# Kernel tuning notes

Hardware: AMD Instinct MI355X
Metric: run time of the kernel (lower is better)

The kernel has to match this reference:

```python
import jax, jax.numpy as jnp
import numpy as np

D_MODEL = 1024
H = 8        # num_heads_kv
G = 8        # num_groups_q (must equal H for the original matmul to be valid)
DEPTH = D_MODEL // H  # 128, depth_q == depth_kv
NEG_INF = jnp.float32(-1e9)


def setup_inputs() -> dict:
    key = jax.random.key(0)
    ks = jax.random.split(key, 7)
    B, Lq, Lk = 2, 2048, 2048
    w_scale = 0.02
    return {
        "x_q": jax.random.normal(ks[0], (B, Lq, D_MODEL), jnp.float32),
        "x_k": jax.random.normal(ks[1], (B, Lk, D_MODEL), jnp.float32),
        "x_v": jax.random.normal(ks[2], (B, Lk, D_MODEL), jnp.float32),
        "Wq": jax.random.normal(ks[3], (D_MODEL, D_MODEL), jnp.float32) * w_scale,
        "Wk": jax.random.normal(ks[4], (D_MODEL, D_MODEL), jnp.float32) * w_scale,
        "Wv": jax.random.normal(ks[5], (D_MODEL, D_MODEL), jnp.float32) * w_scale,
        "Wo": jax.random.normal(ks[6], (D_MODEL, D_MODEL), jnp.float32) * w_scale,
        "mask": jnp.ones((B, 1, Lq, Lk), jnp.bool_),
    }


def reference(x_q, x_k, x_v, Wq, Wk, Wv, Wo, mask):
    B, Lq, _ = x_q.shape
    Lk = x_k.shape[1]
    # nn.Linear: y = x @ W.T (no bias)
    q = (x_q @ Wq.T).reshape(B, Lq, G, DEPTH).transpose(0, 2, 1, 3)  # (B,G,Lq,D)
    k = (x_k @ Wk.T).reshape(B, Lk, H, DEPTH).transpose(0, 2, 1, 3)  # (B,H,Lk,D)
    v = (x_v @ Wv.T).reshape(B, Lk, H, DEPTH).transpose(0, 2, 1, 3)  # (B,H,Lk,D)
    scale = 1.0 / np.sqrt(DEPTH).astype(np.float32)

    def attend(q_g):  # q_g: (B,Lq,D), one query group broadcast over all KV heads
        s = jnp.einsum("bqd,bhkd->bhqk", q_g, k) * scale       # (B,H,Lq,Lk)
        s = jnp.where(mask, s, NEG_INF)                          # masked_fill(mask==0, -inf)
        w = jax.nn.softmax(s, axis=-1)
        o = jnp.einsum("bhqk,bhkd->bhqd", w, v)                 # (B,H,Lq,D)
        return o.mean(axis=1)                                    # mean over kv heads -> (B,Lq,D)

    # sequential over groups (matches original Python loop; bounds peak memory)
    out_g = jax.lax.map(attend, jnp.moveaxis(q, 1, 0))           # (G,B,Lq,D)
    combined = jnp.moveaxis(out_g, 0, 2).reshape(B, Lq, G * DEPTH)
    return combined @ Wo.T
```

## Files before the change

### kernel.cpp

```cpp
#include <hip/hip_runtime.h>
#include <type_traits>
#include <utility>


using u16 = unsigned short;

typedef float f32x4 __attribute__((ext_vector_type(4)));
typedef short short8 __attribute__((ext_vector_type(8)));
typedef __bf16 bf16x8 __attribute__((ext_vector_type(8)));

#define DEV __device__ __forceinline__

template <typename V, typename = void> struct MfmaTakes : std::false_type {};
template <typename V>
struct MfmaTakes<V, std::void_t<decltype(__builtin_amdgcn_mfma_f32_16x16x32_bf16(
    std::declval<V>(), std::declval<V>(), std::declval<f32x4>(), 0, 0, 0))>>
    : std::true_type {};
using mfma_ab = std::conditional_t<MfmaTakes<short8>::value, short8, bf16x8>;
static_assert(sizeof(mfma_ab) == 16, "mfma operand must be 4 VGPRs");

DEV f32x4 mfma16x16(short8 a, short8 b, f32x4 c) {
  return __builtin_amdgcn_mfma_f32_16x16x32_bf16(
      __builtin_bit_cast(mfma_ab, a), __builtin_bit_cast(mfma_ab, b), c, 0, 0, 0);
}

DEV u16 f2b(float f) {
  unsigned u = __float_as_uint(f);
  u += 0x7fffu + ((u >> 16) & 1u);
  return (u16)(u >> 16);
}
DEV float b2f(u16 h) { return __uint_as_float(((unsigned)h) << 16); }

DEV short8 ld8(const u16* p) { return *reinterpret_cast<const short8*>(p); }
DEV void st8(u16* p, short8 v) { *reinterpret_cast<short8*>(p) = v; }

__global__ __launch_bounds__(256) void k_cvt(const float* __restrict__ src,
                                             u16* __restrict__ dst, int n4) {
  int i = blockIdx.x * 256 + threadIdx.x;
  if (i >= n4) return;
  float4 v = reinterpret_cast<const float4*>(src)[i];
  unsigned long long r = (unsigned long long)f2b(v.x) |
                         ((unsigned long long)f2b(v.y) << 16) |
                         ((unsigned long long)f2b(v.z) << 32) |
                         ((unsigned long long)f2b(v.w) << 48);
  reinterpret_cast<unsigned long long*>(dst)[i] = r;
}

template <typename AT, typename OutT>
__global__ __launch_bounds__(256) void k_gemm_nt(const AT* __restrict__ A,
                                                 const u16* __restrict__ Bm,
                                                 OutT* __restrict__ C,
                                                 int M, int N, int K) {
  __shared__ __align__(16) u16 As[128][40];
  __shared__ __align__(16) u16 Bs[128][40];
  const int tid = threadIdx.x, lane = tid & 63, w = tid >> 6;
  const int lr = lane & 15, lg = lane >> 4;
  const int wr = w >> 1, wc = w & 1;
  const int m0 = blockIdx.y * 128, n0 = blockIdx.x * 128;

  f32x4 acc[4][4];
#pragma unroll
  for (int mi = 0; mi < 4; ++mi)
#pragma unroll
    for (int ni = 0; ni < 4; ++ni) acc[mi][ni] = f32x4{0.f, 0.f, 0.f, 0.f};

  for (int k0 = 0; k0 < K; k0 += 32) {
#pragma unroll
    for (int i = 0; i < 2; ++i) {
      int c = tid + i * 256;
      int r = c >> 2, j = c & 3;
      short8 va;
      if constexpr (std::is_same_v<AT, float>) {
        const float* ap = A + (size_t)(m0 + r) * K + k0 + j * 8;
        float4 f0 = *reinterpret_cast<const float4*>(ap);
        float4 f1 = *reinterpret_cast<const float4*>(ap + 4);
        va = short8{(short)f2b(f0.x), (short)f2b(f0.y), (short)f2b(f0.z), (short)f2b(f0.w),
                    (short)f2b(f1.x), (short)f2b(f1.y), (short)f2b(f1.z), (short)f2b(f1.w)};
      } else {
        va = ld8(A + (size_t)(m0 + r) * K + k0 + j * 8);
      }
      short8 vb = ld8(Bm + (size_t)(n0 + r) * K + k0 + j * 8);
      st8(&As[r][j * 8], va);
      st8(&Bs[r][j * 8], vb);
    }
    __syncthreads();
    short8 af[4], bf[4];
#pragma unroll
    for (int mi = 0; mi < 4; ++mi) af[mi] = ld8(&As[wr * 64 + mi * 16 + lr][lg * 8]);
#pragma unroll
    for (int ni = 0; ni < 4; ++ni) bf[ni] = ld8(&Bs[wc * 64 + ni * 16 + lr][lg * 8]);
#pragma unroll
    for (int mi = 0; mi < 4; ++mi)
#pragma unroll
      for (int ni = 0; ni < 4; ++ni)
        acc[mi][ni] = mfma16x16(af[mi], bf[ni], acc[mi][ni]);
    __syncthreads();
  }
#pragma unroll
  for (int mi = 0; mi < 4; ++mi)
#pragma unroll
    for (int ni = 0; ni < 4; ++ni)
#pragma unroll
      for (int r = 0; r < 4; ++r) {
        int row = m0 + wr * 64 + mi * 16 + lg * 4 + r;
        int col = n0 + wc * 64 + ni * 16 + lr;
        if constexpr (std::is_same_v<OutT, float>)
          C[(size_t)row * N + col] = acc[mi][ni][r];
        else
          C[(size_t)row * N + col] = f2b(acc[mi][ni][r]);
      }
}

__global__ __launch_bounds__(256) void k_transpose_v(const u16* __restrict__ V,
                                                     u16* __restrict__ Vt) {
  int bid = blockIdx.x;
  int lt = bid & 31, dt = (bid >> 5) & 1, bh = bid >> 6;
  int b = bh >> 3, h = bh & 7;
  __shared__ u16 t[64][72];
#pragma unroll
  for (int i = 0; i < 16; ++i) {
    int idx = threadIdx.x + i * 256;
    int r = idx >> 6, c = idx & 63;
    t[r][c] = V[(size_t)(b * 2048 + lt * 64 + r) * 1024 + h * 128 + dt * 64 + c];
  }
  __syncthreads();
#pragma unroll
  for (int i = 0; i < 16; ++i) {
    int idx = threadIdx.x + i * 256;
    int r = idx >> 6, c = idx & 63;
    Vt[(size_t)(bh * 128 + dt * 64 + r) * 2048 + lt * 64 + c] = t[c][r];
  }
}

__global__ __launch_bounds__(256) void k_attn(const u16* __restrict__ Q,
                                              const u16* __restrict__ K,
                                              const u16* __restrict__ Vt,
                                              float* __restrict__ Cacc) {
  const int bid = blockIdx.x;
  const int qt = bid & 31, g = (bid >> 5) & 7, b = (bid >> 8) & 1, h = (bid >> 9) & 7;
  const int tid = threadIdx.x, lane = tid & 63, w = tid >> 6;
  const int lr = lane & 15, lg = lane >> 4;

  __shared__ __align__(16) u16 ks[64 * 128];
  __shared__ __align__(16) u16 vts[128 * 64];
  __shared__ __align__(16) u16 ps[4 * 16 * 64];

  auto KS = [&](int row, int e) -> u16* { return &ks[row * 128 + (e ^ ((row & 7) << 3))]; };
  auto VT = [&](int row, int e) -> u16* { return &vts[row * 64 + (e ^ ((row & 7) << 3))]; };
  auto PS = [&](int ww, int row, int e) -> u16* {
    return &ps[ww * 1024 + row * 64 + (e ^ ((row & 7) << 3))];
  };

  const int q0 = qt * 64;

  short8 qf[4];
  {
    const u16* qp = Q + (size_t)(b * 2048 + q0 + w * 16 + lr) * 1024 + g * 128;
    const float sc = 0.08838834764831845f;
#pragma unroll
    for (int kf = 0; kf < 4; ++kf) {
      short8 v = ld8(qp + kf * 32 + lg * 8);
#pragma unroll
      for (int e = 0; e < 8; ++e) v[e] = (short)f2b(b2f((u16)v[e]) * sc);
      qf[kf] = v;
    }
  }

  const short one_bf = (short)0x3F80;
  const short8 ones = short8{one_bf, one_bf, one_bf, one_bf, one_bf, one_bf, one_bf, one_bf};

  f32x4 oh[8];
#pragma unroll
  for (int f = 0; f < 8; ++f) oh[f] = f32x4{0.f, 0.f, 0.f, 0.f};
  f32x4 lsum = f32x4{0.f, 0.f, 0.f, 0.f};
  float mrun[4] = {-1e30f, -1e30f, -1e30f, -1e30f};

  for (int kt = 0; kt < 32; ++kt) {
    const int k0 = kt * 64;
#pragma unroll
    for (int i = 0; i < 4; ++i) {
      int c = tid + i * 256;
      {
        int r = c >> 4, j = c & 15;
        st8(KS(r, j * 8), ld8(K + (size_t)(b * 2048 + k0 + r) * 1024 + h * 128 + j * 8));
      }
      {
        int d = c >> 3, j = c & 7;
        st8(VT(d, j * 8), ld8(Vt + (size_t)((b * 8 + h) * 128 + d) * 2048 + k0 + j * 8));
      }
    }
    __syncthreads();

    f32x4 s[4];
#pragma unroll
    for (int c = 0; c < 4; ++c) {
      s[c] = f32x4{0.f, 0.f, 0.f, 0.f};
#pragma unroll
      for (int kf = 0; kf < 4; ++kf) {
        short8 bfr = ld8(KS(c * 16 + lr, kf * 32 + lg * 8));
        s[c] = mfma16x16(qf[kf], bfr, s[c]);
      }
    }

    float vmax[4];
    bool grow = false;
#pragma unroll
    for (int r = 0; r < 4; ++r) {
      float v = fmaxf(fmaxf(s[0][r], s[1][r]), fmaxf(s[2][r], s[3][r]));
#pragma unroll
      for (int off = 1; off <= 8; off <<= 1) v = fmaxf(v, __shfl_xor(v, off));
      vmax[r] = v;
      grow = grow || (v > mrun[r]);
    }
    if (__any(grow)) {
#pragma unroll
      for (int r = 0; r < 4; ++r) {
        float mn = fmaxf(mrun[r], vmax[r]);
        float corr = __expf(mrun[r] - mn);
        mrun[r] = mn;
        lsum[r] *= corr;
#pragma unroll
        for (int f = 0; f < 8; ++f) oh[f][r] *= corr;
      }
    }
#pragma unroll
    for (int c = 0; c < 4; ++c)
#pragma unroll
      for (int r = 0; r < 4; ++r) {
        float p = __expf(s[c][r] - mrun[r]);
        *PS(w, lg * 4 + r, c * 16 + lr) = __builtin_bit_cast(u16, (__bf16)p);
      }
    asm volatile("s_waitcnt lgkmcnt(0)" ::: "memory");
    __builtin_amdgcn_sched_barrier(0);

    short8 p0 = ld8(PS(w, lr, lg * 8));
    short8 p1 = ld8(PS(w, lr, 32 + lg * 8));
    lsum = mfma16x16(p0, ones, lsum);
    lsum = mfma16x16(p1, ones, lsum);
#pragma unroll
    for (int f = 0; f < 8; ++f) {
      short8 v0 = ld8(VT(f * 16 + lr, lg * 8));
      short8 v1 = ld8(VT(f * 16 + lr, 32 + lg * 8));
      oh[f] = mfma16x16(p0, v0, oh[f]);
      oh[f] = mfma16x16(p1, v1, oh[f]);
    }
    __syncthreads();
  }

  float norm[4];
#pragma unroll
  for (int r = 0; r < 4; ++r) norm[r] = 0.125f / lsum[r];
  float* co = Cacc + (size_t)(b * 2048 + q0 + w * 16 + lg * 4) * 1024 + g * 128 + lr;
#pragma unroll
  for (int f = 0; f < 8; ++f)
#pragma unroll
    for (int r = 0; r < 4; ++r)
      atomicAdd(&co[(size_t)r * 1024 + f * 16], oh[f][r] * norm[r]);
}

extern "C" void kernel_launch(void* const* d_in, const int* in_sizes, int n_in,
                              void* d_out, int out_size, void* d_ws, size_t ws_size,
                              hipStream_t stream) {
  const float* x_q = (const float*)d_in[0];
  const float* x_k = (const float*)d_in[1];
  const float* x_v = (const float*)d_in[2];
  const float* Wq = (const float*)d_in[3];
  const float* Wk = (const float*)d_in[4];
  const float* Wv = (const float*)d_in[5];
  const float* Wo = (const float*)d_in[6];
  float* out = (float*)d_out;

  const size_t NX = (size_t)2 * 2048 * 1024;
  const size_t NW = (size_t)1024 * 1024;
  u16* ws = (u16*)d_ws;
  u16* xqb = ws;
  u16* xkb = xqb + NX;
  u16* xvb = xkb + NX;
  u16* wqb = xvb + NX;
  u16* wkb = wqb + NW;
  u16* wvb = wkb + NW;
  u16* wob = wvb + NW;
  u16* Qb  = wob + NW;
  u16* Kb  = Qb + NX;
  u16* Vb  = Kb + NX;
  u16* Vtb = xqb;
  float* Cacc = (float*)xkb;

  dim3 blk(256);
  k_cvt<<<dim3(NX / 1024), blk, 0, stream>>>(x_q, xqb, (int)(NX / 4));
  k_cvt<<<dim3(NX / 1024), blk, 0, stream>>>(x_k, xkb, (int)(NX / 4));
  k_cvt<<<dim3(NX / 1024), blk, 0, stream>>>(x_v, xvb, (int)(NX / 4));
  k_cvt<<<dim3(NW / 1024), blk, 0, stream>>>(Wq, wqb, (int)(NW / 4));
  k_cvt<<<dim3(NW / 1024), blk, 0, stream>>>(Wk, wkb, (int)(NW / 4));
  k_cvt<<<dim3(NW / 1024), blk, 0, stream>>>(Wv, wvb, (int)(NW / 4));
  k_cvt<<<dim3(NW / 1024), blk, 0, stream>>>(Wo, wob, (int)(NW / 4));

  dim3 ggrid(8, 32);
  k_gemm_nt<u16, u16><<<ggrid, blk, 0, stream>>>(xqb, wqb, Qb, 4096, 1024, 1024);
  k_gemm_nt<u16, u16><<<ggrid, blk, 0, stream>>>(xkb, wkb, Kb, 4096, 1024, 1024);
  k_gemm_nt<u16, u16><<<ggrid, blk, 0, stream>>>(xvb, wvb, Vb, 4096, 1024, 1024);

  k_transpose_v<<<dim3(1024), blk, 0, stream>>>(Vb, Vtb);

  hipMemsetAsync(Cacc, 0, NX * sizeof(float), stream);
  k_attn<<<dim3(4096), blk, 0, stream>>>(Qb, Kb, Vtb, Cacc);

  k_gemm_nt<float, float><<<ggrid, blk, 0, stream>>>(Cacc, wob, out, 4096, 1024, 1024);
}
```

Measured before the change: 886.6 us.

## Double query rows per attention block and prefetch K/V tiles via registers

Each attention block now handles 128 query rows (32 per wave, two 16-row MFMA tiles), so every K/V tile staged in LDS is reused twice as often and the grid is halved. The next K/V tile is loaded from global memory into registers while the current tile is being computed, then written to LDS after a barrier, to overlap load latency with compute. The softmax scale is folded with log2(e) so exp2f can replace __expf. The cost is more accumulator registers and reduced occupancy, plus an extra barrier per iteration.

Result: slower. 1.275 ms (+43.8%).

```diff
diff --git a/kernel.cpp b/kernel.cpp
--- a/kernel.cpp
+++ b/kernel.cpp
@@ -137,125 +137,162 @@
                                               const u16* __restrict__ Vt,
                                               float* __restrict__ Cacc) {
   const int bid = blockIdx.x;
-  const int qt = bid & 31, g = (bid >> 5) & 7, b = (bid >> 8) & 1, h = (bid >> 9) & 7;
+  const int qt = bid & 15, g = (bid >> 4) & 7, b = (bid >> 7) & 1, h = (bid >> 8) & 7;
   const int tid = threadIdx.x, lane = tid & 63, w = tid >> 6;
   const int lr = lane & 15, lg = lane >> 4;
 
   __shared__ __align__(16) u16 ks[64 * 128];
   __shared__ __align__(16) u16 vts[128 * 64];
-  __shared__ __align__(16) u16 ps[4 * 16 * 64];
+  __shared__ __align__(16) u16 ps[4 * 32 * 64];
 
   auto KS = [&](int row, int e) -> u16* { return &ks[row * 128 + (e ^ ((row & 7) << 3))]; };
   auto VT = [&](int row, int e) -> u16* { return &vts[row * 64 + (e ^ ((row & 7) << 3))]; };
   auto PS = [&](int ww, int row, int e) -> u16* {
-    return &ps[ww * 1024 + row * 64 + (e ^ ((row & 7) << 3))];
+    return &ps[ww * 2048 + row * 64 + (e ^ ((row & 7) << 3))];
   };
 
-  const int q0 = qt * 64;
-
-  short8 qf[4];
+  const int q0 = qt * 128;
+  const u16* Kbase = K + (size_t)b * 2048 * 1024 + h * 128;
+  const u16* Vtbase = Vt + (size_t)((b * 8 + h) * 128) * 2048;
+
+  short8 qf[2][4];
   {
-    const u16* qp = Q + (size_t)(b * 2048 + q0 + w * 16 + lr) * 1024 + g * 128;
-    const float sc = 0.08838834764831845f;
-#pragma unroll
-    for (int kf = 0; kf < 4; ++kf) {
-      short8 v = ld8(qp + kf * 32 + lg * 8);
-#pragma unroll
-      for (int e = 0; e < 8; ++e) v[e] = (short)f2b(b2f((u16)v[e]) * sc);
-      qf[kf] = v;
+    const float sc = 0.08838834764831845f * 1.4426950408889634f;
+#pragma unroll
+    for (int m = 0; m < 2; ++m) {
+      const u16* qp = Q + (size_t)(b * 2048 + q0 + w * 32 + m * 16 + lr) * 1024 + g * 128;
+#pragma unroll
+      for (int kf = 0; kf < 4; ++kf) {
+        short8 v = ld8(qp + kf * 32 + lg * 8);
+#pragma unroll
+        for (int e = 0; e < 8; ++e) v[e] = (short)f2b(b2f((u16)v[e]) * sc);
+        qf[m][kf] = v;
+      }
     }
   }
 
   const short one_bf = (short)0x3F80;
   const short8 ones = short8{one_bf, one_bf, one_bf, one_bf, one_bf, one_bf, one_bf, one_bf};
 
-  f32x4 oh[8];
-#pragma unroll
-  for (int f = 0; f < 8; ++f) oh[f] = f32x4{0.f, 0.f, 0.f, 0.f};
-  f32x4 lsum = f32x4{0.f, 0.f, 0.f, 0.f};
-  float mrun[4] = {-1e30f, -1e30f, -1e30f, -1e30f};
-
-  for (int kt = 0; kt < 32; ++kt) {
+  f32x4 oh[2][8];
+#pragma unroll
+  for (int m = 0; m < 2; ++m)
+#pragma unroll
+    for (int f = 0; f < 8; ++f) oh[m][f] = f32x4{0.f, 0.f, 0.f, 0.f};
+  f32x4 lsum[2] = {f32x4{0.f, 0.f, 0.f, 0.f}, f32x4{0.f, 0.f, 0.f, 0.f}};
+  float mrun[2][4] = {{-1e30f, -1e30f, -1e30f, -1e30f}, {-1e30f, -1e30f, -1e30f, -1e30f}};
+
+  short8 kreg[4], vreg[4];
+  auto LOAD = [&](int kt) {
     const int k0 = kt * 64;
 #pragma unroll
     for (int i = 0; i < 4; ++i) {
       int c = tid + i * 256;
-      {
-        int r = c >> 4, j = c & 15;
-        st8(KS(r, j * 8), ld8(K + (size_t)(b * 2048 + k0 + r) * 1024 + h * 128 + j * 8));
-      }
-      {
-        int d = c >> 3, j = c & 7;
-        st8(VT(d, j * 8), ld8(Vt + (size_t)((b * 8 + h) * 128 + d) * 2048 + k0 + j * 8));
-      }
-    }
-    __syncthreads();
-
-    f32x4 s[4];
-#pragma unroll
-    for (int c = 0; c < 4; ++c) {
-      s[c] = f32x4{0.f, 0.f, 0.f, 0.f};
+      kreg[i] = ld8(Kbase + (size_t)(k0 + (c >> 4)) * 1024 + (c & 15) * 8);
+      vreg[i] = ld8(Vtbase + (size_t)(c >> 3) * 2048 + k0 + (c & 7) * 8);
+    }
+  };
+  auto WRITE = [&]() {
+#pragma unroll
+    for (int i = 0; i < 4; ++i) {
+      int c = tid + i * 256;
+      st8(KS(c >> 4, (c & 15) * 8), kreg[i]);
+      st8(VT(c >> 3, (c & 7) * 8), vreg[i]);
+    }
+  };
+
+  LOAD(0);
+  WRITE();
+  __syncthreads();
+
+  for (int kt = 0; kt < 32; ++kt) {
+    if (kt < 31) LOAD(kt + 1);
+
+    f32x4 s[2][4];
+#pragma unroll
+    for (int m = 0; m < 2; ++m)
+#pragma unroll
+      for (int c = 0; c < 4; ++c) s[m][c] = f32x4{0.f, 0.f, 0.f, 0.f};
+#pragma unroll
+    for (int c = 0; c < 4; ++c)
 #pragma unroll
       for (int kf = 0; kf < 4; ++kf) {
         short8 bfr = ld8(KS(c * 16 + lr, kf * 32 + lg * 8));
-        s[c] = mfma16x16(qf[kf], bfr, s[c]);
-      }
-    }
-
-    float vmax[4];
+        s[0][c] = mfma16x16(qf[0][kf], bfr, s[0][c]);
+        s[1][c] = mfma16x16(qf[1][kf], bfr, s[1][c]);
+      }
+
+    float vmax[2][4];
     bool grow = false;
 #pragma unroll
-    for (int r = 0; r < 4; ++r) {
-      float v = fmaxf(fmaxf(s[0][r], s[1][r]), fmaxf(s[2][r], s[3][r]));
-#pragma unroll
-      for (int off = 1; off <= 8; off <<= 1) v = fmaxf(v, __shfl_xor(v, off));
-      vmax[r] = v;
-      grow = grow || (v > mrun[r]);
-    }
+    for (int m = 0; m < 2; ++m)
+#pragma unroll
+      for (int r = 0; r < 4; ++r) {
+        float v = fmaxf(fmaxf(s[m][0][r], s[m][1][r]), fmaxf(s[m][2][r], s[m][3][r]));
+#pragma unroll
+        for (int off = 1; off <= 8; off <<= 1) v = fmaxf(v, __shfl_xor(v, off));
+        vmax[m][r] = v;
+        grow = grow || (v > mrun[m][r]);
+      }
     if (__any(grow)) {
 #pragma unroll
-      for (int r = 0; r < 4; ++r) {
-        float mn = fmaxf(mrun[r], vmax[r]);
-        float corr = __expf(mrun[r] - mn);
-        mrun[r] = mn;
-        lsum[r] *= corr;
-#pragma unroll
-        for (int f = 0; f < 8; ++f) oh[f][r] *= corr;
-      }
-    }
-#pragma unroll
-    for (int c = 0; c < 4; ++c)
-#pragma unroll
-      for (int r = 0; r < 4; ++r) {
-        float p = __expf(s[c][r] - mrun[r]);
-        *PS(w, lg * 4 + r, c * 16 + lr) = __builtin_bit_cast(u16, (__bf16)p);
-      }
+      for (int m = 0; m < 2; ++m)
+#pragma unroll
+        for (int r = 0; r < 4; ++r) {
+          float mn = fmaxf(mrun[m][r], vmax[m][r]);
+          float corr = exp2f(mrun[m][r] - mn);
+          mrun[m][r] = mn;
+          lsum[m][r] *= corr;
+#pragma unroll
+          for (int f = 0; f < 8; ++f) oh[m][f][r] *= corr;
+        }
+    }
+#pragma unroll
+    for (int m = 0; m < 2; ++m)
+#pragma unroll
+      for (int c = 0; c < 4; ++c)
+#pragma unroll
+        for (int r = 0; r < 4; ++r) {
+          float p = exp2f(s[m][c][r] - mrun[m][r]);
+          *PS(w, m * 16 + lg * 4 + r, c * 16 + lr) = __builtin_bit_cast(u16, (__bf16)p);
+        }
     asm volatile("s_waitcnt lgkmcnt(0)" ::: "memory");
     __builtin_amdgcn_sched_barrier(0);
 
-    short8 p0 = ld8(PS(w, lr, lg * 8));
-    short8 p1 = ld8(PS(w, lr, 32 + lg * 8));
-    lsum = mfma16x16(p0, ones, lsum);
-    lsum = mfma16x16(p1, ones, lsum);
+    short8 p0[2], p1[2];
+#pragma unroll
+    for (int m = 0; m < 2; ++m) {
+      p0[m] = ld8(PS(w, m * 16 + lr, lg * 8));
+      p1[m] = ld8(PS(w, m * 16 + lr, 32 + lg * 8));
+      lsum[m] = mfma16x16(p0[m], ones, lsum[m]);
+      lsum[m] = mfma16x16(p1[m], ones, lsum[m]);
+    }
 #pragma unroll
     for (int f = 0; f < 8; ++f) {
       short8 v0 = ld8(VT(f * 16 + lr, lg * 8));
       short8 v1 = ld8(VT(f * 16 + lr, 32 + lg * 8));
-      oh[f] = mfma16x16(p0, v0, oh[f]);
-      oh[f] = mfma16x16(p1, v1, oh[f]);
+      oh[0][f] = mfma16x16(p0[0], v0, oh[0][f]);
+      oh[0][f] = mfma16x16(p1[0], v1, oh[0][f]);
+      oh[1][f] = mfma16x16(p0[1], v0, oh[1][f]);
+      oh[1][f] = mfma16x16(p1[1], v1, oh[1][f]);
     }
     __syncthreads();
-  }
-
-  float norm[4];
-#pragma unroll
-  for (int r = 0; r < 4; ++r) norm[r] = 0.125f / lsum[r];
-  float* co = Cacc + (size_t)(b * 2048 + q0 + w * 16 + lg * 4) * 1024 + g * 128 + lr;
-#pragma unroll
-  for (int f = 0; f < 8; ++f)
-#pragma unroll
-    for (int r = 0; r < 4; ++r)
-      atomicAdd(&co[(size_t)r * 1024 + f * 16], oh[f][r] * norm[r]);
+    if (kt < 31) WRITE();
+    __syncthreads();
+  }
+
+#pragma unroll
+  for (int m = 0; m < 2; ++m) {
+    float norm[4];
+#pragma unroll
+    for (int r = 0; r < 4; ++r) norm[r] = 0.125f / lsum[m][r];
+    float* co = Cacc + (size_t)(b * 2048 + q0 + w * 32 + m * 16 + lg * 4) * 1024 + g * 128 + lr;
+#pragma unroll
+    for (int f = 0; f < 8; ++f)
+#pragma unroll
+      for (int r = 0; r < 4; ++r)
+        atomicAdd(&co[(size_t)r * 1024 + f * 16], oh[m][f][r] * norm[r]);
+  }
 }
 
 extern "C" void kernel_launch(void* const* d_in, const int* in_sizes, int n_in,
@@ -303,7 +340,7 @@
   k_transpose_v<<<dim3(1024), blk, 0, stream>>>(Vb, Vtb);
 
   hipMemsetAsync(Cacc, 0, NX * sizeof(float), stream);
-  k_attn<<<dim3(4096), blk, 0, stream>>>(Qb, Kb, Vtb, Cacc);
+  k_attn<<<dim3(2048), blk, 0, stream>>>(Qb, Kb, Vtb, Cacc);
 
   k_gemm_nt<float, float><<<ggrid, blk, 0, stream>>>(Cacc, wob, out, 4096, 1024, 1024);
 }
```
